# Performance work log

Hardware: AMD Instinct MI355X
Metric: run time of the kernel (lower is better)

The kernel has to match this reference:

```python
import jax, jax.numpy as jnp
import numpy as np

N = 20000          # nodes
E = 200000         # edges
IN = 256           # in_channels
OUT = 256          # out_channels (heads * per-head)
H = 2              # heads
C = OUT // 2       # per-head channels (out_channels // 2)
TDIM = 100         # time_enc.out_channels
MSG = 156          # msg_dim
EDGE_DIM = TDIM + MSG  # 256
P = 0.1            # dropout prob


def setup_inputs() -> dict:
    key = jax.random.key(0)
    ks = jax.random.split(key, 20)
    s = 1.0 / np.sqrt(IN)
    se = 1.0 / np.sqrt(EDGE_DIM)
    return {
        "x": jax.random.normal(ks[0], (N, IN), jnp.float32),
        "last_update": jax.random.uniform(ks[1], (N,), jnp.float32) * 100.0,
        "edge_index": jax.random.randint(ks[2], (2, E), 0, N, jnp.int64),
        "t": jax.random.uniform(ks[3], (E,), jnp.float32) * 100.0,
        "msg": jax.random.normal(ks[4], (E, MSG), jnp.float32),
        "u_edge": jax.random.uniform(ks[5], (E,), jnp.float32),
        "u_attn": jax.random.uniform(ks[6], (E, H), jnp.float32),
        # TimeEncoder: cos(Linear(1, TDIM))
        "time_w": jax.random.normal(ks[7], (TDIM,), jnp.float32),
        "time_b": jax.random.normal(ks[8], (TDIM,), jnp.float32) * 0.1,
        # TransformerConv params ([in, out] layout)
        "Wq": jax.random.normal(ks[9], (IN, H * C), jnp.float32) * s,
        "bq": jnp.zeros((H * C,), jnp.float32),
        "Wk": jax.random.normal(ks[10], (IN, H * C), jnp.float32) * s,
        "bk": jnp.zeros((H * C,), jnp.float32),
        "Wv": jax.random.normal(ks[11], (IN, H * C), jnp.float32) * s,
        "bv": jnp.zeros((H * C,), jnp.float32),
        "We": jax.random.normal(ks[12], (EDGE_DIM, H * C), jnp.float32) * se,
        "be": jnp.zeros((H * C,), jnp.float32),
        "Ws": jax.random.normal(ks[13], (IN, H * C), jnp.float32) * s,
        "bs": jnp.zeros((H * C,), jnp.float32),
    }


def reference(x, last_update, edge_index, t, msg, u_edge, u_attn,
              time_w, time_b, Wq, bq, Wk, bk, Wv, bv, We, be, Ws, bs):
    src, dst = edge_index[0], edge_index[1]
    # time encoding of relative time (TGN TimeEncoder: cos(Linear(1, TDIM)))
    rel_t = last_update[src] - t                              # [E]
    rel_enc = jnp.cos(rel_t[:, None] * time_w[None, :] + time_b)  # [E, TDIM]
    edge_attr = jnp.concatenate([rel_enc, msg], axis=-1)      # [E, EDGE_DIM]
    # dropout_adj: drop edges with prob P (no rescale)
    keep = u_edge > P                                         # [E] bool

    q = (x @ Wq + bq).reshape(N, H, C)
    k = (x @ Wk + bk).reshape(N, H, C)
    v = (x @ Wv + bv).reshape(N, H, C)
    e = (edge_attr @ We + be).reshape(E, H, C)

    kj = k[src] + e                                           # [E, H, C]
    alpha = jnp.einsum('ehc,ehc->eh', q[dst], kj) / jnp.sqrt(jnp.float32(C))
    alpha = jnp.where(keep[:, None], alpha, -jnp.inf)
    # segment softmax over incoming edges of each dst node
    m = jax.ops.segment_max(alpha, dst, num_segments=N)       # [N, H]
    m = jnp.where(jnp.isfinite(m), m, 0.0)
    ex = jnp.where(keep[:, None], jnp.exp(alpha - m[dst]), 0.0)
    denom = jax.ops.segment_sum(ex, dst, num_segments=N)      # [N, H]
    attn = ex / (denom[dst] + 1e-16)                          # [E, H]
    # attention dropout (post-softmax, inverted scaling)
    attn = attn * (u_attn > P).astype(attn.dtype) / (1.0 - P)

    msg_out = (v[src] + e) * attn[:, :, None]                 # [E, H, C]
    out = jax.ops.segment_sum(msg_out, dst, num_segments=N).reshape(N, H * C)
    # root/skip connection
    return out + (x @ Ws + bs)
```

## Files before the change

kernel.cpp:

```cpp
#include <hip/hip_runtime.h>

#define NND 20000
#define NE 200000
#define PDROP 0.1f

typedef unsigned short u16;
typedef __bf16 bf16x8 __attribute__((ext_vector_type(8)));
typedef float f32x4 __attribute__((ext_vector_type(4)));

__device__ __forceinline__ float b2f(u16 u) {
  unsigned v = ((unsigned)u) << 16;
  float f;
  __builtin_memcpy(&f, &v, 4);
  return f;
}
__device__ __forceinline__ u16 f2b(float f) {
  unsigned x;
  __builtin_memcpy(&x, &f, 4);
  unsigned r = x + 0x7fffu + ((x >> 16) & 1u);
  return (u16)(r >> 16);
}

__global__ void convert_x(const float* __restrict__ x, u16* __restrict__ xb) {
  int i = blockIdx.x * blockDim.x + threadIdx.x;
  if (i < NND * 256 / 4) {
    float4 v = ((const float4*)x)[i];
    ushort4 o;
    o.x = f2b(v.x); o.y = f2b(v.y); o.z = f2b(v.z); o.w = f2b(v.w);
    ((ushort4*)xb)[i] = o;
  }
}

struct WTArgs {
  const float* W[6];
  u16* WT[6];
};
__global__ void convert_wT(WTArgs a) {
  int gid = blockIdx.x * blockDim.x + threadIdx.x;
  if (gid >= 6 * 65536) return;
  int w = gid >> 16, r = gid & 65535;
  if (w < 5) {
    int n = r >> 8, k = r & 255;
    a.WT[w][n * 256 + k] = f2b(a.W[w][k * 256 + n]);
  } else {
    a.WT[5][r] = f2b(a.W[5][r]);
  }
}

__global__ void zero2(int* __restrict__ cnt, int* __restrict__ cur) {
  int i = blockIdx.x * blockDim.x + threadIdx.x;
  if (i < NND) { cnt[i] = 0; cur[i] = 0; }
}
__global__ void csr_count(const int* __restrict__ ei, int* __restrict__ cnt) {
  int e = blockIdx.x * blockDim.x + threadIdx.x;
  if (e < NE) atomicAdd(&cnt[ei[NE + e]], 1);
}
__global__ __launch_bounds__(1024) void scan_rowptr(const int* __restrict__ cnt,
                                                    int* __restrict__ rowptr) {
  __shared__ int sums[1024];
  const int tid = threadIdx.x;
  const int base = tid * 20;
  int local[20];
  int run = 0;
#pragma unroll
  for (int i = 0; i < 20; i++) {
    int idx = base + i;
    local[i] = run;
    run += (idx < NND) ? cnt[idx] : 0;
  }
  sums[tid] = run;
  __syncthreads();
  for (int off = 1; off < 1024; off <<= 1) {
    int v = (tid >= off) ? sums[tid - off] : 0;
    __syncthreads();
    sums[tid] += v;
    __syncthreads();
  }
  int prev = (tid > 0) ? sums[tid - 1] : 0;
#pragma unroll
  for (int i = 0; i < 20; i++) {
    int idx = base + i;
    if (idx < NND) rowptr[idx] = prev + local[i];
  }
  if (tid == 1023) rowptr[NND] = sums[1023];
}
__global__ void csr_fill(const int* __restrict__ ei,
                         const float* __restrict__ last_update,
                         const float* __restrict__ t,
                         const float* __restrict__ u_edge,
                         const float* __restrict__ u_attn,
                         const int* __restrict__ rowptr, int* __restrict__ cur,
                         int* __restrict__ pos, uint4* __restrict__ recs) {
  int e = blockIdx.x * blockDim.x + threadIdx.x;
  if (e < NE) {
    int s = ei[e];
    int d = ei[NE + e];
    int p = rowptr[d] + atomicAdd(&cur[d], 1);
    pos[e] = p;
    bool keep = u_edge[e] > PDROP;
    float rt = last_update[s] - t[e];
    float2 ua = *(const float2*)&u_attn[(size_t)e * 2];
    uint4 r;
    r.x = (unsigned)s | (keep ? 0u : 0x80000000u);
    r.y = __float_as_uint(rt);
    r.z = __float_as_uint(ua.x > PDROP ? (1.f / 0.9f) : 0.f);
    r.w = __float_as_uint(ua.y > PDROP ? (1.f / 0.9f) : 0.f);
    recs[p] = r;
  }
}

__global__ void msgs_fill(const float* __restrict__ msg,
                          const int* __restrict__ pos, u16* __restrict__ msgs) {
  int i = blockIdx.x * blockDim.x + threadIdx.x;
  if (i >= NE * 39) return;
  int e = i / 39;
  int c = (i - e * 39) * 4;
  float4 v = *(const float4*)&msg[(size_t)e * 156 + c];
  ushort4 o;
  o.x = f2b(v.x); o.y = f2b(v.y); o.z = f2b(v.z); o.w = f2b(v.w);
  *(ushort4*)&msgs[(size_t)pos[e] * 156 + c] = o;
}

__device__ __forceinline__ void mfma_tile(const u16 (*As)[72], const u16 (*Bs)[72],
                                          f32x4 acc[4][4], int wm, int wn,
                                          int fr, int fg) {
#pragma unroll
  for (int ks = 0; ks < 2; ks++) {
    bf16x8 a[4], b[4];
#pragma unroll
    for (int i = 0; i < 4; i++)
      a[i] = *(const bf16x8*)&As[wm * 64 + i * 16 + fr][ks * 32 + fg * 8];
#pragma unroll
    for (int j = 0; j < 4; j++)
      b[j] = *(const bf16x8*)&Bs[wn * 64 + j * 16 + fr][ks * 32 + fg * 8];
#pragma unroll
    for (int i = 0; i < 4; i++)
#pragma unroll
      for (int j = 0; j < 4; j++)
        acc[i][j] = __builtin_amdgcn_mfma_f32_16x16x32_bf16(a[i], b[j], acc[i][j], 0, 0, 0);
  }
}

struct NodeArgs {
  const u16* BT[4];
  const float* bias[4];
  u16* outb[3];
  float* outf;
};
__global__ __launch_bounds__(256) void gemm_node(const u16* __restrict__ xb,
                                                 NodeArgs args) {
  __shared__ __attribute__((aligned(16))) u16 As[128][72];
  __shared__ __attribute__((aligned(16))) u16 Bs[128][72];
  const int tid = threadIdx.x;
  const int w = blockIdx.y >> 1;
  const int col0 = (blockIdx.y & 1) * 128;
  const int row0 = blockIdx.x * 128;
  const u16* BT = args.BT[w];
  const float* bias = args.bias[w];
  const int wid = tid >> 6, lane = tid & 63;
  const int wm = wid >> 1, wn = wid & 1;
  const int fr = lane & 15, fg = lane >> 4;
  f32x4 acc[4][4] = {};
  for (int k0 = 0; k0 < 256; k0 += 64) {
#pragma unroll
    for (int i = 0; i < 4; i++) {
      int idx = tid + i * 256;
      int row = idx >> 3, vc = idx & 7;
      int g = row0 + row;
      uint4 v = make_uint4(0, 0, 0, 0);
      if (g < NND) v = *(const uint4*)&xb[(size_t)g * 256 + k0 + vc * 8];
      *(uint4*)&As[row][vc * 8] = v;
      *(uint4*)&Bs[row][vc * 8] = *(const uint4*)&BT[(size_t)(col0 + row) * 256 + k0 + vc * 8];
    }
    __syncthreads();
    mfma_tile(As, Bs, acc, wm, wn, fr, fg);
    __syncthreads();
  }
#pragma unroll
  for (int mi = 0; mi < 4; mi++) {
#pragma unroll
    for (int rr = 0; rr < 4; rr++) {
      int grow = row0 + wm * 64 + mi * 16 + fg * 4 + rr;
      if (grow >= NND) continue;
#pragma unroll
      for (int ni = 0; ni < 4; ni++) {
        int gcol = col0 + wn * 64 + ni * 16 + fr;
        float val = acc[mi][ni][rr] + bias[gcol];
        if (w < 3)
          args.outb[w][(size_t)grow * 256 + gcol] = f2b(val);
        else
          args.outf[(size_t)grow * 256 + gcol] = val;
      }
    }
  }
}

__global__ __launch_bounds__(256) void gemm_qwe(const u16* __restrict__ qb,
                                                const u16* __restrict__ Web,
                                                u16* __restrict__ qWeb) {
  __shared__ __attribute__((aligned(16))) u16 As[128][72];
  __shared__ __attribute__((aligned(16))) u16 Bs[128][72];
  const int tid = threadIdx.x;
  const int h = blockIdx.y >> 1;
  const int col0 = (blockIdx.y & 1) * 128;
  const int row0 = blockIdx.x * 128;
  const int wid = tid >> 6, lane = tid & 63;
  const int wm = wid >> 1, wn = wid & 1;
  const int fr = lane & 15, fg = lane >> 4;
  f32x4 acc[4][4] = {};
  for (int k0 = 0; k0 < 128; k0 += 64) {
#pragma unroll
    for (int i = 0; i < 4; i++) {
      int idx = tid + i * 256;
      int row = idx >> 3, vc = idx & 7;
      int g = row0 + row;
      uint4 v = make_uint4(0, 0, 0, 0);
      if (g < NND) v = *(const uint4*)&qb[(size_t)g * 256 + h * 128 + k0 + vc * 8];
      *(uint4*)&As[row][vc * 8] = v;
      *(uint4*)&Bs[row][vc * 8] =
          *(const uint4*)&Web[(size_t)(col0 + row) * 256 + h * 128 + k0 + vc * 8];
    }
    __syncthreads();
    mfma_tile(As, Bs, acc, wm, wn, fr, fg);
    __syncthreads();
  }
#pragma unroll
  for (int mi = 0; mi < 4; mi++) {
#pragma unroll
    for (int rr = 0; rr < 4; rr++) {
      int grow = row0 + wm * 64 + mi * 16 + fg * 4 + rr;
      if (grow >= NND) continue;
#pragma unroll
      for (int ni = 0; ni < 4; ni++) {
        int gj = col0 + wn * 64 + ni * 16 + fr;
        qWeb[(size_t)grow * 512 + h * 256 + gj] = f2b(acc[mi][ni][rr]);
      }
    }
  }
}

__global__ __launch_bounds__(256) void node_fused(
    const u16* __restrict__ qb, const u16* __restrict__ kb,
    const u16* __restrict__ vb, const u16* __restrict__ qWeb,
    const u16* __restrict__ msgs, const float* __restrict__ tw,
    const float* __restrict__ tb_, const float* __restrict__ be,
    const int* __restrict__ rowptr, const uint4* __restrict__ recs,
    u16* __restrict__ aggb, float* __restrict__ out) {
  const int node = (blockIdx.x * blockDim.x + threadIdx.x) >> 6;
  const int lane = threadIdx.x & 63;
  if (node >= NND) return;
  const int beg = rowptr[node], end = rowptr[node + 1];
  const int c0 = lane * 4, hl = lane >> 5;

  ushort4 q4 = *(const ushort4*)&qb[(size_t)node * 256 + c0];
  float qf0 = b2f(q4.x), qf1 = b2f(q4.y), qf2 = b2f(q4.z), qf3 = b2f(q4.w);
  ushort4 w0v = *(const ushort4*)&qWeb[(size_t)node * 512 + c0];
  ushort4 w1v = *(const ushort4*)&qWeb[(size_t)node * 512 + 256 + c0];
  float qw00 = b2f(w0v.x), qw01 = b2f(w0v.y), qw02 = b2f(w0v.z), qw03 = b2f(w0v.w);
  float qw10 = b2f(w1v.x), qw11 = b2f(w1v.y), qw12 = b2f(w1v.z), qw13 = b2f(w1v.w);
  float4 bev = *(const float4*)&be[c0];
  float pb = qf0 * bev.x + qf1 * bev.y + qf2 * bev.z + qf3 * bev.w;
#pragma unroll
  for (int off = 16; off; off >>= 1) pb += __shfl_xor(pb, off);
  float tw0 = 0, tw1 = 0, tw2 = 0, tw3 = 0, tb0 = 0, tb1 = 0, tb2 = 0, tb3 = 0;
  if (c0 < 100) {
    float4 a = *(const float4*)&tw[c0];
    float4 b = *(const float4*)&tb_[c0];
    tw0 = a.x; tw1 = a.y; tw2 = a.z; tw3 = a.w;
    tb0 = b.x; tb1 = b.y; tb2 = b.z; tb3 = b.w;
  }
  const float inv = 0.08838834764831845f;

  float m0 = -INFINITY, m1 = -INFINITY;
  float den0 = 0.f, den1 = 0.f, sw0 = 0.f, sw1 = 0.f;
  float vc0 = 0, vc1 = 0, vc2 = 0, vc3 = 0;
  float g00 = 0, g01 = 0, g02 = 0, g03 = 0;
  float g10 = 0, g11 = 0, g12 = 0, g13 = 0;

  for (int j0 = beg; j0 < end; j0 += 4) {
    float ea[4][4];
    unsigned se[4];
    float rt[4], wk0[4], wk1[4];
    ushort4 k4[4], v4[4], mm4[4];
#pragma unroll
    for (int e = 0; e < 4; ++e) {
      int j = j0 + e;
      int jc = (j < end) ? j : (end - 1);
      uint4 rr = recs[jc];
      bool valid = (j < end);
      se[e] = valid ? rr.x : 0xFFFFFFFFu;
      rt[e] = __uint_as_float(rr.y);
      wk0[e] = valid ? __uint_as_float(rr.z) : 0.f;
      wk1[e] = valid ? __uint_as_float(rr.w) : 0.f;
      int s_ = (int)(rr.x & 0x7fffffffu);
      k4[e] = *(const ushort4*)&kb[(size_t)s_ * 256 + c0];
      v4[e] = *(const ushort4*)&vb[(size_t)s_ * 256 + c0];
      if (c0 >= 100)
        mm4[e] = *(const ushort4*)&msgs[(size_t)jc * 156 + (c0 - 100)];
    }
    if (c0 < 100) {
#pragma unroll
      for (int e = 0; e < 4; ++e) {
        ea[e][0] = __cosf(rt[e] * tw0 + tb0);
        ea[e][1] = __cosf(rt[e] * tw1 + tb1);
        ea[e][2] = __cosf(rt[e] * tw2 + tb2);
        ea[e][3] = __cosf(rt[e] * tw3 + tb3);
      }
    } else {
#pragma unroll
      for (int e = 0; e < 4; ++e) {
        ea[e][0] = b2f(mm4[e].x); ea[e][1] = b2f(mm4[e].y);
        ea[e][2] = b2f(mm4[e].z); ea[e][3] = b2f(mm4[e].w);
      }
    }
    float z[4], pq[4];
#pragma unroll
    for (int e = 0; e < 4; ++e) {
      pq[e] = qf0 * b2f(k4[e].x) + qf1 * b2f(k4[e].y) +
              qf2 * b2f(k4[e].z) + qf3 * b2f(k4[e].w);
      float pe0 = qw00 * ea[e][0] + qw01 * ea[e][1] + qw02 * ea[e][2] + qw03 * ea[e][3];
      float pe1 = qw10 * ea[e][0] + qw11 * ea[e][1] + qw12 * ea[e][2] + qw13 * ea[e][3];
      float y0 = pe0 + __shfl_xor(pe0, 32);
      float y1 = pe1 + __shfl_xor(pe1, 32);
      z[e] = (lane < 32) ? y0 : y1;
    }
#pragma unroll
    for (int off = 16; off; off >>= 1) {
#pragma unroll
      for (int e = 0; e < 4; ++e) {
        z[e] += __shfl_xor(z[e], off);
        pq[e] += __shfl_xor(pq[e], off);
      }
    }
    float a0[4], a1[4];
#pragma unroll
    for (int e = 0; e < 4; ++e) {
      float a = (se[e] < 0x80000000u) ? (pq[e] + z[e] + pb) * inv : -INFINITY;
      float aoth = __shfl_xor(a, 32);
      a0[e] = (lane < 32) ? a : aoth;
      a1[e] = (lane < 32) ? aoth : a;
    }
    float cm0 = fmaxf(fmaxf(a0[0], a0[1]), fmaxf(a0[2], a0[3]));
    float cm1 = fmaxf(fmaxf(a1[0], a1[1]), fmaxf(a1[2], a1[3]));
    if (cm0 > m0) {
      float sc = (m0 > -1e30f) ? __expf(m0 - cm0) : 0.f;
      den0 *= sc; sw0 *= sc;
      g00 *= sc; g01 *= sc; g02 *= sc; g03 *= sc;
      float scv = hl ? 1.f : sc;
      vc0 *= scv; vc1 *= scv; vc2 *= scv; vc3 *= scv;
      m0 = cm0;
    }
    if (cm1 > m1) {
      float sc = (m1 > -1e30f) ? __expf(m1 - cm1) : 0.f;
      den1 *= sc; sw1 *= sc;
      g10 *= sc; g11 *= sc; g12 *= sc; g13 *= sc;
      float scv = hl ? sc : 1.f;
      vc0 *= scv; vc1 *= scv; vc2 *= scv; vc3 *= scv;
      m1 = cm1;
    }
#pragma unroll
    for (int e = 0; e < 4; ++e) {
      float ex0 = (a0[e] > -1e30f) ? __expf(a0[e] - m0) : 0.f;
      float ex1 = (a1[e] > -1e30f) ? __expf(a1[e] - m1) : 0.f;
      den0 += ex0; den1 += ex1;
      float w0 = ex0 * wk0[e], w1 = ex1 * wk1[e];
      float wv = hl ? w1 : w0;
      vc0 += wv * b2f(v4[e].x); vc1 += wv * b2f(v4[e].y);
      vc2 += wv * b2f(v4[e].z); vc3 += wv * b2f(v4[e].w);
      g00 += w0 * ea[e][0]; g01 += w0 * ea[e][1];
      g02 += w0 * ea[e][2]; g03 += w0 * ea[e][3];
      g10 += w1 * ea[e][0]; g11 += w1 * ea[e][1];
      g12 += w1 * ea[e][2]; g13 += w1 * ea[e][3];
      sw0 += w0; sw1 += w1;
    }
  }

  float rden0 = 1.f / (den0 + 1e-16f), rden1 = 1.f / (den1 + 1e-16f);
  float rv = hl ? rden1 : rden0;
  float swv = hl ? sw1 : sw0;
  float4 o = *(float4*)&out[(size_t)node * 256 + c0];
  o.x += (vc0 + swv * bev.x) * rv;
  o.y += (vc1 + swv * bev.y) * rv;
  o.z += (vc2 + swv * bev.z) * rv;
  o.w += (vc3 + swv * bev.w) * rv;
  *(float4*)&out[(size_t)node * 256 + c0] = o;
  ushort4 a0v, a1v;
  a0v.x = f2b(g00 * rden0); a0v.y = f2b(g01 * rden0);
  a0v.z = f2b(g02 * rden0); a0v.w = f2b(g03 * rden0);
  a1v.x = f2b(g10 * rden1); a1v.y = f2b(g11 * rden1);
  a1v.z = f2b(g12 * rden1); a1v.w = f2b(g13 * rden1);
  *(ushort4*)&aggb[(size_t)node * 256 + c0] = a0v;
  *(ushort4*)&aggb[(size_t)(NND + node) * 256 + c0] = a1v;
}

__global__ __launch_bounds__(256) void gemm_final(const u16* __restrict__ aggb,
                                                  const u16* __restrict__ WeT,
                                                  float* __restrict__ out) {
  __shared__ __attribute__((aligned(16))) u16 As[128][72];
  __shared__ __attribute__((aligned(16))) u16 Bs[128][72];
  const int tid = threadIdx.x;
  const int h = blockIdx.y;
  const int row0 = blockIdx.x * 128;
  const u16* A = aggb + (size_t)h * NND * 256;
  const int wid = tid >> 6, lane = tid & 63;
  const int wm = wid >> 1, wn = wid & 1;
  const int fr = lane & 15, fg = lane >> 4;
  f32x4 acc[4][4] = {};
  for (int k0 = 0; k0 < 256; k0 += 64) {
#pragma unroll
    for (int i = 0; i < 4; i++) {
      int idx = tid + i * 256;
      int row = idx >> 3, vc = idx & 7;
      int g = row0 + row;
      uint4 v = make_uint4(0, 0, 0, 0);
      if (g < NND) v = *(const uint4*)&A[(size_t)g * 256 + k0 + vc * 8];
      *(uint4*)&As[row][vc * 8] = v;
      *(uint4*)&Bs[row][vc * 8] =
          *(const uint4*)&WeT[(size_t)(h * 128 + row) * 256 + k0 + vc * 8];
    }
    __syncthreads();
    mfma_tile(As, Bs, acc, wm, wn, fr, fg);
    __syncthreads();
  }
#pragma unroll
  for (int mi = 0; mi < 4; mi++) {
#pragma unroll
    for (int rr = 0; rr < 4; rr++) {
      int grow = row0 + wm * 64 + mi * 16 + fg * 4 + rr;
      if (grow >= NND) continue;
#pragma unroll
      for (int ni = 0; ni < 4; ni++) {
        int gcol = wn * 64 + ni * 16 + fr;
        out[(size_t)grow * 256 + h * 128 + gcol] += acc[mi][ni][rr];
      }
    }
  }
}

extern "C" void kernel_launch(void* const* d_in, const int* in_sizes, int n_in,
                              void* d_out, int out_size, void* d_ws, size_t ws_size,
                              hipStream_t stream) {
  const float* x = (const float*)d_in[0];
  const float* last_update = (const float*)d_in[1];
  const int* ei = (const int*)d_in[2];
  const float* t = (const float*)d_in[3];
  const float* msg = (const float*)d_in[4];
  const float* u_edge = (const float*)d_in[5];
  const float* u_attn = (const float*)d_in[6];
  const float* time_w = (const float*)d_in[7];
  const float* time_b = (const float*)d_in[8];
  const float* Wq = (const float*)d_in[9];
  const float* bq = (const float*)d_in[10];
  const float* Wk = (const float*)d_in[11];
  const float* bk = (const float*)d_in[12];
  const float* Wv = (const float*)d_in[13];
  const float* bv = (const float*)d_in[14];
  const float* We = (const float*)d_in[15];
  const float* be = (const float*)d_in[16];
  const float* Ws = (const float*)d_in[17];
  const float* bs = (const float*)d_in[18];
  float* out = (float*)d_out;

  char* ws = (char*)d_ws;
  u16* xb = (u16*)(ws + 0);
  u16* WT0 = (u16*)(ws + 10240000);
  u16* qb = (u16*)(ws + 11026432);
  u16* kb = (u16*)(ws + 21266432);
  u16* vb = (u16*)(ws + 31506432);
  u16* qWeb = (u16*)(ws + 41746432);
  u16* aggb = (u16*)(ws + 62226432);
  uint4* recs = (uint4*)(ws + 82706432);
  u16* msgs = (u16*)(ws + 85906432);
  int* pos = (int*)(ws + 148306432);
  int* cnt = (int*)(ws + 149106432);
  int* cur = (int*)(ws + 149186432);
  int* rowptr = (int*)(ws + 149266432);

  zero2<<<(NND + 255) / 256, 256, 0, stream>>>(cnt, cur);
  csr_count<<<(NE + 255) / 256, 256, 0, stream>>>(ei, cnt);
  scan_rowptr<<<1, 1024, 0, stream>>>(cnt, rowptr);
  csr_fill<<<(NE + 255) / 256, 256, 0, stream>>>(ei, last_update, t, u_edge,
                                                 u_attn, rowptr, cur, pos, recs);

  msgs_fill<<<(NE * 39 + 255) / 256, 256, 0, stream>>>(msg, pos, msgs);

  WTArgs wa;
  wa.W[0] = Wq; wa.W[1] = Wk; wa.W[2] = Wv; wa.W[3] = Ws; wa.W[4] = We; wa.W[5] = We;
  for (int i = 0; i < 6; i++) wa.WT[i] = WT0 + (size_t)i * 65536;
  convert_wT<<<(6 * 65536 + 255) / 256, 256, 0, stream>>>(wa);
  convert_x<<<(NND * 64 + 255) / 256, 256, 0, stream>>>(x, xb);

  NodeArgs na;
  na.BT[0] = wa.WT[0]; na.BT[1] = wa.WT[1]; na.BT[2] = wa.WT[2]; na.BT[3] = wa.WT[3];
  na.bias[0] = bq; na.bias[1] = bk; na.bias[2] = bv; na.bias[3] = bs;
  na.outb[0] = qb; na.outb[1] = kb; na.outb[2] = vb;
  na.outf = out;
  dim3 gn((NND + 127) / 128, 8);
  gemm_node<<<gn, 256, 0, stream>>>(xb, na);

  dim3 gq((NND + 127) / 128, 4);
  gemm_qwe<<<gq, 256, 0, stream>>>(qb, wa.WT[5], qWeb);

  node_fused<<<(NND + 3) / 4, 256, 0, stream>>>(
      qb, kb, vb, qWeb, msgs, time_w, time_b, be, rowptr, recs, aggb, out);

  dim3 gf((NND + 127) / 128, 2);
  gemm_final<<<gf, 256, 0, stream>>>(aggb, wa.WT[4], out);
}
```

Baseline: 256.0 us.

## Merge prep kernels, fuse msg scatter into csr_fill, combine shuffle reductions

Fuses convert_x, convert_wT and zero2 into one prep launch, and folds msgs_fill into csr_fill using one wavefront per edge, so the pos buffer round trip goes away. Also sums the q·k and q·e partial dot products before the cross-lane reduction, which halves the shuffles in node_fused. The costs are fewer launches and less index traffic. In exchange csr_fill launches 64 threads per edge with 25 of them idle, and lane 0 serially does the atomic before the others can write.

New measurement: 268.5 us. 4.9% more time.

```diff
diff --git a/kernel.cpp b/kernel.cpp
--- a/kernel.cpp
+++ b/kernel.cpp
@@ -21,36 +21,37 @@
   return (u16)(r >> 16);
 }
 
-__global__ void convert_x(const float* __restrict__ x, u16* __restrict__ xb) {
-  int i = blockIdx.x * blockDim.x + threadIdx.x;
-  if (i < NND * 256 / 4) {
+struct WTArgs {
+  const float* W[6];
+  u16* WT[6];
+};
+
+__global__ __launch_bounds__(256) void prep(const float* __restrict__ x,
+                                            u16* __restrict__ xb, WTArgs a,
+                                            int* __restrict__ cnt,
+                                            int* __restrict__ cur) {
+  const int b = blockIdx.x, tid = threadIdx.x;
+  if (b < 5000) {
+    int i = b * 256 + tid;
     float4 v = ((const float4*)x)[i];
     ushort4 o;
     o.x = f2b(v.x); o.y = f2b(v.y); o.z = f2b(v.z); o.w = f2b(v.w);
     ((ushort4*)xb)[i] = o;
-  }
-}
-
-struct WTArgs {
-  const float* W[6];
-  u16* WT[6];
-};
-__global__ void convert_wT(WTArgs a) {
-  int gid = blockIdx.x * blockDim.x + threadIdx.x;
-  if (gid >= 6 * 65536) return;
-  int w = gid >> 16, r = gid & 65535;
-  if (w < 5) {
-    int n = r >> 8, k = r & 255;
-    a.WT[w][n * 256 + k] = f2b(a.W[w][k * 256 + n]);
+  } else if (b < 6536) {
+    int gid = (b - 5000) * 256 + tid;
+    int w = gid >> 16, r = gid & 65535;
+    if (w < 5) {
+      int n = r >> 8, k = r & 255;
+      a.WT[w][n * 256 + k] = f2b(a.W[w][k * 256 + n]);
+    } else {
+      a.WT[5][r] = f2b(a.W[5][r]);
+    }
   } else {
-    a.WT[5][r] = f2b(a.W[5][r]);
-  }
-}
-
-__global__ void zero2(int* __restrict__ cnt, int* __restrict__ cur) {
-  int i = blockIdx.x * blockDim.x + threadIdx.x;
-  if (i < NND) { cnt[i] = 0; cur[i] = 0; }
-}
+    int i = (b - 6536) * 256 + tid;
+    if (i < NND) { cnt[i] = 0; cur[i] = 0; }
+  }
+}
+
 __global__ void csr_count(const int* __restrict__ ei, int* __restrict__ cnt) {
   int e = blockIdx.x * blockDim.x + threadIdx.x;
   if (e < NE) atomicAdd(&cnt[ei[NE + e]], 1);
@@ -84,19 +85,21 @@
   }
   if (tid == 1023) rowptr[NND] = sums[1023];
 }
-__global__ void csr_fill(const int* __restrict__ ei,
-                         const float* __restrict__ last_update,
-                         const float* __restrict__ t,
-                         const float* __restrict__ u_edge,
-                         const float* __restrict__ u_attn,
-                         const int* __restrict__ rowptr, int* __restrict__ cur,
-                         int* __restrict__ pos, uint4* __restrict__ recs) {
-  int e = blockIdx.x * blockDim.x + threadIdx.x;
-  if (e < NE) {
+
+__global__ __launch_bounds__(256) void csr_fill(
+    const int* __restrict__ ei, const float* __restrict__ last_update,
+    const float* __restrict__ t, const float* __restrict__ u_edge,
+    const float* __restrict__ u_attn, const float* __restrict__ msg,
+    const int* __restrict__ rowptr, int* __restrict__ cur,
+    uint4* __restrict__ recs, u16* __restrict__ msgs) {
+  int e = (blockIdx.x * blockDim.x + threadIdx.x) >> 6;
+  int lane = threadIdx.x & 63;
+  if (e >= NE) return;
+  int p = 0;
+  if (lane == 0) {
     int s = ei[e];
     int d = ei[NE + e];
-    int p = rowptr[d] + atomicAdd(&cur[d], 1);
-    pos[e] = p;
+    p = rowptr[d] + atomicAdd(&cur[d], 1);
     bool keep = u_edge[e] > PDROP;
     float rt = last_update[s] - t[e];
     float2 ua = *(const float2*)&u_attn[(size_t)e * 2];
@@ -107,18 +110,14 @@
     r.w = __float_as_uint(ua.y > PDROP ? (1.f / 0.9f) : 0.f);
     recs[p] = r;
   }
-}
-
-__global__ void msgs_fill(const float* __restrict__ msg,
-                          const int* __restrict__ pos, u16* __restrict__ msgs) {
-  int i = blockIdx.x * blockDim.x + threadIdx.x;
-  if (i >= NE * 39) return;
-  int e = i / 39;
-  int c = (i - e * 39) * 4;
-  float4 v = *(const float4*)&msg[(size_t)e * 156 + c];
-  ushort4 o;
-  o.x = f2b(v.x); o.y = f2b(v.y); o.z = f2b(v.z); o.w = f2b(v.w);
-  *(ushort4*)&msgs[(size_t)pos[e] * 156 + c] = o;
+  p = __shfl(p, 0);
+  int c = lane * 4;
+  if (c < 156) {
+    float4 v = *(const float4*)&msg[(size_t)e * 156 + c];
+    ushort4 o;
+    o.x = f2b(v.x); o.y = f2b(v.y); o.z = f2b(v.z); o.w = f2b(v.w);
+    *(ushort4*)&msgs[(size_t)p * 156 + c] = o;
+  }
 }
 
 __device__ __forceinline__ void mfma_tile(const u16 (*As)[72], const u16 (*Bs)[72],
@@ -313,29 +312,26 @@
         ea[e][2] = b2f(mm4[e].z); ea[e][3] = b2f(mm4[e].w);
       }
     }
-    float z[4], pq[4];
+    float zq[4];
 #pragma unroll
     for (int e = 0; e < 4; ++e) {
-      pq[e] = qf0 * b2f(k4[e].x) + qf1 * b2f(k4[e].y) +
-              qf2 * b2f(k4[e].z) + qf3 * b2f(k4[e].w);
+      float pq = qf0 * b2f(k4[e].x) + qf1 * b2f(k4[e].y) +
+                 qf2 * b2f(k4[e].z) + qf3 * b2f(k4[e].w);
       float pe0 = qw00 * ea[e][0] + qw01 * ea[e][1] + qw02 * ea[e][2] + qw03 * ea[e][3];
       float pe1 = qw10 * ea[e][0] + qw11 * ea[e][1] + qw12 * ea[e][2] + qw13 * ea[e][3];
       float y0 = pe0 + __shfl_xor(pe0, 32);
       float y1 = pe1 + __shfl_xor(pe1, 32);
-      z[e] = (lane < 32) ? y0 : y1;
+      zq[e] = ((lane < 32) ? y0 : y1) + pq;
     }
 #pragma unroll
     for (int off = 16; off; off >>= 1) {
 #pragma unroll
-      for (int e = 0; e < 4; ++e) {
-        z[e] += __shfl_xor(z[e], off);
-        pq[e] += __shfl_xor(pq[e], off);
-      }
+      for (int e = 0; e < 4; ++e) zq[e] += __shfl_xor(zq[e], off);
     }
     float a0[4], a1[4];
 #pragma unroll
     for (int e = 0; e < 4; ++e) {
-      float a = (se[e] < 0x80000000u) ? (pq[e] + z[e] + pb) * inv : -INFINITY;
+      float a = (se[e] < 0x80000000u) ? (zq[e] + pb) * inv : -INFINITY;
       float aoth = __shfl_xor(a, 32);
       a0[e] = (lane < 32) ? a : aoth;
       a1[e] = (lane < 32) ? aoth : a;
@@ -471,24 +467,19 @@
   u16* aggb = (u16*)(ws + 62226432);
   uint4* recs = (uint4*)(ws + 82706432);
   u16* msgs = (u16*)(ws + 85906432);
-  int* pos = (int*)(ws + 148306432);
-  int* cnt = (int*)(ws + 149106432);
-  int* cur = (int*)(ws + 149186432);
-  int* rowptr = (int*)(ws + 149266432);
-
-  zero2<<<(NND + 255) / 256, 256, 0, stream>>>(cnt, cur);
-  csr_count<<<(NE + 255) / 256, 256, 0, stream>>>(ei, cnt);
-  scan_rowptr<<<1, 1024, 0, stream>>>(cnt, rowptr);
-  csr_fill<<<(NE + 255) / 256, 256, 0, stream>>>(ei, last_update, t, u_edge,
-                                                 u_attn, rowptr, cur, pos, recs);
-
-  msgs_fill<<<(NE * 39 + 255) / 256, 256, 0, stream>>>(msg, pos, msgs);
+  int* cnt = (int*)(ws + 148306432);
+  int* cur = (int*)(ws + 148386432);
+  int* rowptr = (int*)(ws + 148466432);
 
   WTArgs wa;
   wa.W[0] = Wq; wa.W[1] = Wk; wa.W[2] = Wv; wa.W[3] = Ws; wa.W[4] = We; wa.W[5] = We;
   for (int i = 0; i < 6; i++) wa.WT[i] = WT0 + (size_t)i * 65536;
-  convert_wT<<<(6 * 65536 + 255) / 256, 256, 0, stream>>>(wa);
-  convert_x<<<(NND * 64 + 255) / 256, 256, 0, stream>>>(x, xb);
+  prep<<<6615, 256, 0, stream>>>(x, xb, wa, cnt, cur);
+
+  csr_count<<<(NE + 255) / 256, 256, 0, stream>>>(ei, cnt);
+  scan_rowptr<<<1, 1024, 0, stream>>>(cnt, rowptr);
+  csr_fill<<<NE / 4, 256, 0, stream>>>(ei, last_update, t, u_edge, u_attn, msg,
+                                       rowptr, cur, recs, msgs);
 
   NodeArgs na;
   na.BT[0] = wa.WT[0]; na.BT[1] = wa.WT[1]; na.BT[2] = wa.WT[2]; na.BT[3] = wa.WT[3];
```

## Drop msg scatter by edge-id indirection and fuse skip GEMM into final GEMM

Applied to the files above, without the earlier changes.

Message rows are now converted to bf16 in original edge order and read through an edge id packed into the CSR record, which removes the pos array and the scattered msgs_fill pass. The skip projection x@Ws is moved out of the node GEMM into the final GEMM as a second K-loop. The node kernel now writes its value aggregate to a bf16 buffer instead of doing a read-modify-write on the fp32 output. The aim is to cut global memory traffic, at the cost of gathered msg reads in the node kernel and extra bf16 rounding of the value aggregate.

Result: no change. 258.0 us (+0.8%).

```diff
diff --git a/kernel.cpp b/kernel.cpp
--- a/kernel.cpp
+++ b/kernel.cpp
@@ -19,6 +19,11 @@
   __builtin_memcpy(&x, &f, 4);
   unsigned r = x + 0x7fffu + ((x >> 16) & 1u);
   return (u16)(r >> 16);
+}
+
+__global__ void zero2(int* __restrict__ cnt, int* __restrict__ cur) {
+  int i = blockIdx.x * blockDim.x + threadIdx.x;
+  if (i < NND) { cnt[i] = 0; cur[i] = 0; }
 }
 
 __global__ void convert_x(const float* __restrict__ x, u16* __restrict__ xb) {
@@ -47,10 +52,20 @@
   }
 }
 
-__global__ void zero2(int* __restrict__ cnt, int* __restrict__ cur) {
-  int i = blockIdx.x * blockDim.x + threadIdx.x;
-  if (i < NND) { cnt[i] = 0; cur[i] = 0; }
-}
+__global__ __launch_bounds__(256) void msgb_fill(const float* __restrict__ msg,
+                                                 u16* __restrict__ msgb) {
+  int e = (blockIdx.x * blockDim.x + threadIdx.x) >> 6;
+  int lane = threadIdx.x & 63;
+  if (e >= NE) return;
+  int c = lane * 4;
+  if (c < 156) {
+    float4 v = *(const float4*)&msg[(size_t)e * 156 + c];
+    ushort4 o;
+    o.x = f2b(v.x); o.y = f2b(v.y); o.z = f2b(v.z); o.w = f2b(v.w);
+    *(ushort4*)&msgb[(size_t)e * 156 + c] = o;
+  }
+}
+
 __global__ void csr_count(const int* __restrict__ ei, int* __restrict__ cnt) {
   int e = blockIdx.x * blockDim.x + threadIdx.x;
   if (e < NE) atomicAdd(&cnt[ei[NE + e]], 1);
@@ -84,41 +99,30 @@
   }
   if (tid == 1023) rowptr[NND] = sums[1023];
 }
+
 __global__ void csr_fill(const int* __restrict__ ei,
                          const float* __restrict__ last_update,
                          const float* __restrict__ t,
                          const float* __restrict__ u_edge,
                          const float* __restrict__ u_attn,
                          const int* __restrict__ rowptr, int* __restrict__ cur,
-                         int* __restrict__ pos, uint4* __restrict__ recs) {
+                         uint4* __restrict__ recs) {
   int e = blockIdx.x * blockDim.x + threadIdx.x;
   if (e < NE) {
     int s = ei[e];
     int d = ei[NE + e];
     int p = rowptr[d] + atomicAdd(&cur[d], 1);
-    pos[e] = p;
     bool keep = u_edge[e] > PDROP;
     float rt = last_update[s] - t[e];
     float2 ua = *(const float2*)&u_attn[(size_t)e * 2];
     uint4 r;
     r.x = (unsigned)s | (keep ? 0u : 0x80000000u);
     r.y = __float_as_uint(rt);
-    r.z = __float_as_uint(ua.x > PDROP ? (1.f / 0.9f) : 0.f);
-    r.w = __float_as_uint(ua.y > PDROP ? (1.f / 0.9f) : 0.f);
+    r.z = (unsigned)e | ((ua.x > PDROP) ? 0x40000000u : 0u) |
+          ((ua.y > PDROP) ? 0x80000000u : 0u);
+    r.w = 0u;
     recs[p] = r;
   }
-}
-
-__global__ void msgs_fill(const float* __restrict__ msg,
-                          const int* __restrict__ pos, u16* __restrict__ msgs) {
-  int i = blockIdx.x * blockDim.x + threadIdx.x;
-  if (i >= NE * 39) return;
-  int e = i / 39;
-  int c = (i - e * 39) * 4;
-  float4 v = *(const float4*)&msg[(size_t)e * 156 + c];
-  ushort4 o;
-  o.x = f2b(v.x); o.y = f2b(v.y); o.z = f2b(v.z); o.w = f2b(v.w);
-  *(ushort4*)&msgs[(size_t)pos[e] * 156 + c] = o;
 }
 
 __device__ __forceinline__ void mfma_tile(const u16 (*As)[72], const u16 (*Bs)[72],
@@ -142,10 +146,9 @@
 }
 
 struct NodeArgs {
-  const u16* BT[4];
-  const float* bias[4];
+  const u16* BT[3];
+  const float* bias[3];
   u16* outb[3];
-  float* outf;
 };
 __global__ __launch_bounds__(256) void gemm_node(const u16* __restrict__ xb,
                                                  NodeArgs args) {
@@ -185,11 +188,7 @@
 #pragma unroll
       for (int ni = 0; ni < 4; ni++) {
         int gcol = col0 + wn * 64 + ni * 16 + fr;
-        float val = acc[mi][ni][rr] + bias[gcol];
-        if (w < 3)
-          args.outb[w][(size_t)grow * 256 + gcol] = f2b(val);
-        else
-          args.outf[(size_t)grow * 256 + gcol] = val;
+        args.outb[w][(size_t)grow * 256 + gcol] = f2b(acc[mi][ni][rr] + bias[gcol]);
       }
     }
   }
@@ -242,10 +241,10 @@
 __global__ __launch_bounds__(256) void node_fused(
     const u16* __restrict__ qb, const u16* __restrict__ kb,
     const u16* __restrict__ vb, const u16* __restrict__ qWeb,
-    const u16* __restrict__ msgs, const float* __restrict__ tw,
+    const u16* __restrict__ msgb, const float* __restrict__ tw,
     const float* __restrict__ tb_, const float* __restrict__ be,
     const int* __restrict__ rowptr, const uint4* __restrict__ recs,
-    u16* __restrict__ aggb, float* __restrict__ out) {
+    u16* __restrict__ aggb, u16* __restrict__ vaggb) {
   const int node = (blockIdx.x * blockDim.x + threadIdx.x) >> 6;
   const int lane = threadIdx.x & 63;
   if (node >= NND) return;
@@ -290,13 +289,16 @@
       bool valid = (j < end);
       se[e] = valid ? rr.x : 0xFFFFFFFFu;
       rt[e] = __uint_as_float(rr.y);
-      wk0[e] = valid ? __uint_as_float(rr.z) : 0.f;
-      wk1[e] = valid ? __uint_as_float(rr.w) : 0.f;
+      unsigned rz = rr.z;
+      wk0[e] = (valid && (rz & 0x40000000u)) ? (1.f / 0.9f) : 0.f;
+      wk1[e] = (valid && (rz & 0x80000000u)) ? (1.f / 0.9f) : 0.f;
       int s_ = (int)(rr.x & 0x7fffffffu);
       k4[e] = *(const ushort4*)&kb[(size_t)s_ * 256 + c0];
       v4[e] = *(const ushort4*)&vb[(size_t)s_ * 256 + c0];
-      if (c0 >= 100)
-        mm4[e] = *(const ushort4*)&msgs[(size_t)jc * 156 + (c0 - 100)];
+      if (c0 >= 100) {
+        int eid = (int)(rz & 0x3FFFFFFFu);
+        mm4[e] = *(const ushort4*)&msgb[(size_t)eid * 156 + (c0 - 100)];
+      }
     }
     if (c0 < 100) {
 #pragma unroll
@@ -313,29 +315,26 @@
         ea[e][2] = b2f(mm4[e].z); ea[e][3] = b2f(mm4[e].w);
       }
     }
-    float z[4], pq[4];
+    float zq[4];
 #pragma unroll
     for (int e = 0; e < 4; ++e) {
-      pq[e] = qf0 * b2f(k4[e].x) + qf1 * b2f(k4[e].y) +
-              qf2 * b2f(k4[e].z) + qf3 * b2f(k4[e].w);
+      float pq = qf0 * b2f(k4[e].x) + qf1 * b2f(k4[e].y) +
+                 qf2 * b2f(k4[e].z) + qf3 * b2f(k4[e].w);
       float pe0 = qw00 * ea[e][0] + qw01 * ea[e][1] + qw02 * ea[e][2] + qw03 * ea[e][3];
       float pe1 = qw10 * ea[e][0] + qw11 * ea[e][1] + qw12 * ea[e][2] + qw13 * ea[e][3];
       float y0 = pe0 + __shfl_xor(pe0, 32);
       float y1 = pe1 + __shfl_xor(pe1, 32);
-      z[e] = (lane < 32) ? y0 : y1;
+      zq[e] = ((lane < 32) ? y0 : y1) + pq;
     }
 #pragma unroll
     for (int off = 16; off; off >>= 1) {
 #pragma unroll
-      for (int e = 0; e < 4; ++e) {
-        z[e] += __shfl_xor(z[e], off);
-        pq[e] += __shfl_xor(pq[e], off);
-      }
+      for (int e = 0; e < 4; ++e) zq[e] += __shfl_xor(zq[e], off);
     }
     float a0[4], a1[4];
 #pragma unroll
     for (int e = 0; e < 4; ++e) {
-      float a = (se[e] < 0x80000000u) ? (pq[e] + z[e] + pb) * inv : -INFINITY;
+      float a = (se[e] < 0x80000000u) ? (zq[e] + pb) * inv : -INFINITY;
       float aoth = __shfl_xor(a, 32);
       a0[e] = (lane < 32) ? a : aoth;
       a1[e] = (lane < 32) ? aoth : a;
@@ -378,12 +377,12 @@
   float rden0 = 1.f / (den0 + 1e-16f), rden1 = 1.f / (den1 + 1e-16f);
   float rv = hl ? rden1 : rden0;
   float swv = hl ? sw1 : sw0;
-  float4 o = *(float4*)&out[(size_t)node * 256 + c0];
-  o.x += (vc0 + swv * bev.x) * rv;
-  o.y += (vc1 + swv * bev.y) * rv;
-  o.z += (vc2 + swv * bev.z) * rv;
-  o.w += (vc3 + swv * bev.w) * rv;
-  *(float4*)&out[(size_t)node * 256 + c0] = o;
+  ushort4 vg;
+  vg.x = f2b((vc0 + swv * bev.x) * rv);
+  vg.y = f2b((vc1 + swv * bev.y) * rv);
+  vg.z = f2b((vc2 + swv * bev.z) * rv);
+  vg.w = f2b((vc3 + swv * bev.w) * rv);
+  *(ushort4*)&vaggb[(size_t)node * 256 + c0] = vg;
   ushort4 a0v, a1v;
   a0v.x = f2b(g00 * rden0); a0v.y = f2b(g01 * rden0);
   a0v.z = f2b(g02 * rden0); a0v.w = f2b(g03 * rden0);
@@ -393,15 +392,16 @@
   *(ushort4*)&aggb[(size_t)(NND + node) * 256 + c0] = a1v;
 }
 
-__global__ __launch_bounds__(256) void gemm_final(const u16* __restrict__ aggb,
-                                                  const u16* __restrict__ WeT,
-                                                  float* __restrict__ out) {
+__global__ __launch_bounds__(256) void gemm_final2(
+    const u16* __restrict__ xb, const u16* __restrict__ aggb,
+    const u16* __restrict__ WsT, const u16* __restrict__ WeT,
+    const float* __restrict__ bs, const u16* __restrict__ vaggb,
+    float* __restrict__ out) {
   __shared__ __attribute__((aligned(16))) u16 As[128][72];
   __shared__ __attribute__((aligned(16))) u16 Bs[128][72];
   const int tid = threadIdx.x;
   const int h = blockIdx.y;
   const int row0 = blockIdx.x * 128;
-  const u16* A = aggb + (size_t)h * NND * 256;
   const int wid = tid >> 6, lane = tid & 63;
   const int wm = wid >> 1, wn = wid & 1;
   const int fr = lane & 15, fg = lane >> 4;
@@ -413,7 +413,24 @@
       int row = idx >> 3, vc = idx & 7;
       int g = row0 + row;
       uint4 v = make_uint4(0, 0, 0, 0);
-      if (g < NND) v = *(const uint4*)&A[(size_t)g * 256 + k0 + vc * 8];
+      if (g < NND) v = *(const uint4*)&xb[(size_t)g * 256 + k0 + vc * 8];
+      *(uint4*)&As[row][vc * 8] = v;
+      *(uint4*)&Bs[row][vc * 8] =
+          *(const uint4*)&WsT[(size_t)(h * 128 + row) * 256 + k0 + vc * 8];
+    }
+    __syncthreads();
+    mfma_tile(As, Bs, acc, wm, wn, fr, fg);
+    __syncthreads();
+  }
+  const u16* A2 = aggb + (size_t)h * NND * 256;
+  for (int k0 = 0; k0 < 256; k0 += 64) {
+#pragma unroll
+    for (int i = 0; i < 4; i++) {
+      int idx = tid + i * 256;
+      int row = idx >> 3, vc = idx & 7;
+      int g = row0 + row;
+      uint4 v = make_uint4(0, 0, 0, 0);
+      if (g < NND) v = *(const uint4*)&A2[(size_t)g * 256 + k0 + vc * 8];
       *(uint4*)&As[row][vc * 8] = v;
       *(uint4*)&Bs[row][vc * 8] =
           *(const uint4*)&WeT[(size_t)(h * 128 + row) * 256 + k0 + vc * 8];
@@ -431,7 +448,9 @@
 #pragma unroll
       for (int ni = 0; ni < 4; ni++) {
         int gcol = wn * 64 + ni * 16 + fr;
-        out[(size_t)grow * 256 + h * 128 + gcol] += acc[mi][ni][rr];
+        int oc = h * 128 + gcol;
+        out[(size_t)grow * 256 + oc] =
+            acc[mi][ni][rr] + bs[oc] + b2f(vaggb[(size_t)grow * 256 + oc]);
       }
     }
   }
@@ -469,41 +488,41 @@
   u16* vb = (u16*)(ws + 31506432);
   u16* qWeb = (u16*)(ws + 41746432);
   u16* aggb = (u16*)(ws + 62226432);
-  uint4* recs = (uint4*)(ws + 82706432);
-  u16* msgs = (u16*)(ws + 85906432);
-  int* pos = (int*)(ws + 148306432);
-  int* cnt = (int*)(ws + 149106432);
-  int* cur = (int*)(ws + 149186432);
-  int* rowptr = (int*)(ws + 149266432);
+  u16* vaggb = (u16*)(ws + 82706432);
+  uint4* recs = (uint4*)(ws + 92946432);
+  u16* msgb = (u16*)(ws + 96146432);
+  int* cnt = (int*)(ws + 158546432);
+  int* cur = (int*)(ws + 158626432);
+  int* rowptr = (int*)(ws + 158706432);
+
+  WTArgs wa;
+  wa.W[0] = Wq; wa.W[1] = Wk; wa.W[2] = Wv; wa.W[3] = Ws; wa.W[4] = We; wa.W[5] = We;
+  for (int i = 0; i < 6; i++) wa.WT[i] = WT0 + (size_t)i * 65536;
 
   zero2<<<(NND + 255) / 256, 256, 0, stream>>>(cnt, cur);
+  convert_wT<<<(6 * 65536 + 255) / 256, 256, 0, stream>>>(wa);
+  convert_x<<<(NND * 64 + 255) / 256, 256, 0, stream>>>(x, xb);
+  msgb_fill<<<NE / 4, 256, 0, stream>>>(msg, msgb);
+
   csr_count<<<(NE + 255) / 256, 256, 0, stream>>>(ei, cnt);
   scan_rowptr<<<1, 1024, 0, stream>>>(cnt, rowptr);
   csr_fill<<<(NE + 255) / 256, 256, 0, stream>>>(ei, last_update, t, u_edge,
-                                                 u_attn, rowptr, cur, pos, recs);
-
-  msgs_fill<<<(NE * 39 + 255) / 256, 256, 0, stream>>>(msg, pos, msgs);
-
-  WTArgs wa;
-  wa.W[0] = Wq; wa.W[1] = Wk; wa.W[2] = Wv; wa.W[3] = Ws; wa.W[4] = We; wa.W[5] = We;
-  for (int i = 0; i < 6; i++) wa.WT[i] = WT0 + (size_t)i * 65536;
-  convert_wT<<<(6 * 65536 + 255) / 256, 256, 0, stream>>>(wa);
-  convert_x<<<(NND * 64 + 255) / 256, 256, 0, stream>>>(x, xb);
+                                                 u_attn, rowptr, cur, recs);
 
   NodeArgs na;
-  na.BT[0] = wa.WT[0]; na.BT[1] = wa.WT[1]; na.BT[2] = wa.WT[2]; na.BT[3] = wa.WT[3];
-  na.bias[0] = bq; na.bias[1] = bk; na.bias[2] = bv; na.bias[3] = bs;
+  na.BT[0] = wa.WT[0]; na.BT[1] = wa.WT[1]; na.BT[2] = wa.WT[2];
+  na.bias[0] = bq; na.bias[1] = bk; na.bias[2] = bv;
   na.outb[0] = qb; na.outb[1] = kb; na.outb[2] = vb;
-  na.outf = out;
-  dim3 gn((NND + 127) / 128, 8);
+  dim3 gn((NND + 127) / 128, 6);
   gemm_node<<<gn, 256, 0, stream>>>(xb, na);
 
   dim3 gq((NND + 127) / 128, 4);
   gemm_qwe<<<gq, 256, 0, stream>>>(qb, wa.WT[5], qWeb);
 
   node_fused<<<(NND + 3) / 4, 256, 0, stream>>>(
-      qb, kb, vb, qWeb, msgs, time_w, time_b, be, rowptr, recs, aggb, out);
+      qb, kb, vb, qWeb, msgb, time_w, time_b, be, rowptr, recs, aggb, vaggb);
 
   dim3 gf((NND + 127) / 128, 2);
-  gemm_final<<<gf, 256, 0, stream>>>(aggb, wa.WT[4], out);
-}
+  gemm_final2<<<gf, 256, 0, stream>>>(xb, aggb, wa.WT[3], wa.WT[4], bs, vaggb,
+                                      out);
+}
```
